# Kernel optimization log

Hardware: AMD Instinct MI355X
Metric: run time of the kernel (lower is better)

The kernel has to match this reference:

```python
import jax, jax.numpy as jnp
import numpy as np

B, L = 1024, 1024
LP, STRIDE, WIN = 64, 32, 8   # patch_length, patch_stride, window_size
GH, RH, NC = 64, 128, 11      # gnn hidden, rnn hidden, num_classes


def setup_inputs() -> dict:
    key = jax.random.key(0)
    ks = jax.random.split(key, 16)
    def n(k, shape, s=0.1):
        return jax.random.normal(k, shape, dtype=jnp.float32) * s
    z = lambda *s: jnp.zeros(s, jnp.float32)
    return {
        "I": jax.random.normal(ks[0], (B, L), dtype=jnp.float32),
        "Q": jax.random.normal(ks[1], (B, L), dtype=jnp.float32),
        "edge_weights": jax.random.normal(ks[2], (LP, LP), dtype=jnp.float32),
        "Wn1": n(ks[3], (GH, 2)),  "bn1": z(GH),
        "Ws1": n(ks[4], (GH, 2)),  "bs1": z(GH),
        "Wn2": n(ks[5], (GH, GH)), "bn2": z(GH),
        "Ws2": n(ks[6], (GH, GH)), "bs2": z(GH),
        "Wih0": n(ks[7], (4 * RH, GH)), "Whh0": n(ks[8], (4 * RH, RH)),
        "bih0": z(4 * RH), "bhh0": z(4 * RH),
        "Wih1": n(ks[9], (4 * RH, RH)), "Whh1": n(ks[10], (4 * RH, RH)),
        "bih1": z(4 * RH), "bhh1": z(4 * RH),
        "Wc1": n(ks[11], (64, RH)), "bc1": z(64),
        "Wc2": n(ks[12], (NC, 64)), "bc2": z(NC),
    }


def _sage(x, adj, deg_inv, Wn, bn, Ws, bs):
    # x: [B,P,Lp,d]; adj: [Lp,Lp]; mean-aggregate neighbors then self+neigh linear + relu
    neigh = jnp.einsum('ij,bpjd->bpid', adj, x) * deg_inv
    return jax.nn.relu(jnp.einsum('bpid,od->bpio', x, Ws) + bs
                       + jnp.einsum('bpid,od->bpio', neigh, Wn) + bn)


def _lstm(x, Wih, Whh, bih, bhh):
    # x: [B,T,D]; PyTorch gate order i,f,g,o
    Hd = Whh.shape[1]
    xg = jnp.einsum('btd,gd->btg', x, Wih) + bih + bhh  # [B,T,4H]
    h0 = jnp.zeros((x.shape[0], Hd), x.dtype)
    def step(carry, xt):
        h, c = carry
        g = xt + h @ Whh.T
        i, f, gg, o = jnp.split(g, 4, axis=-1)
        c = jax.nn.sigmoid(f) * c + jax.nn.sigmoid(i) * jnp.tanh(gg)
        h = jax.nn.sigmoid(o) * jnp.tanh(c)
        return (h, c), h
    (h, _), hs = jax.lax.scan(step, (h0, h0), jnp.swapaxes(xg, 0, 1))
    return jnp.swapaxes(hs, 0, 1), h


def _forward(I, Q, edge_weights, Wn1, bn1, Ws1, bs1, Wn2, bn2, Ws2, bs2,
             Wih0, Whh0, bih0, bhh0, Wih1, Whh1, bih1, bhh1, Wc1, bc1, Wc2, bc2):
    Lp = edge_weights.shape[0]
    P = (I.shape[-1] - Lp) // STRIDE + 1
    # vectorized patch extraction: [B,P,Lp,2]
    idx = jnp.arange(P)[:, None] * STRIDE + jnp.arange(Lp)[None, :]
    patches = jnp.stack([I[:, idx], Q[:, idx]], axis=-1)
    # banded adjacency shared across all patches
    r = jnp.arange(Lp)
    mask = ((jnp.abs(r[:, None] - r[None, :]) <= WIN) & (r[:, None] != r[None, :])).astype(jnp.float32)
    adj = jax.nn.sigmoid(edge_weights) * mask
    deg = adj.sum(axis=1, keepdims=True)           # [Lp,1]
    deg_inv = jnp.where(deg > 0, 1.0 / deg, 0.0)
    x = _sage(patches, adj, deg_inv, Wn1, bn1, Ws1, bs1)   # [B,P,Lp,GH]
    x = _sage(x, adj, deg_inv, Wn2, bn2, Ws2, bs2)
    feats = x.sum(axis=2)                                  # [B,P,GH]
    out0, _ = _lstm(feats, Wih0, Whh0, bih0, bhh0)
    _, h = _lstm(out0, Wih1, Whh1, bih1, bhh1)             # last layer final hidden [B,RH]
    hid = jax.nn.relu(h @ Wc1.T + bc1)
    return hid @ Wc2.T + bc2                               # [B,NC]


def reference(I, Q, edge_weights, Wn1, bn1, Ws1, bs1, Wn2, bn2, Ws2, bs2,
              Wih0, Whh0, bih0, bhh0, Wih1, Whh1, bih1, bhh1, Wc1, bc1, Wc2, bc2):
    return _forward(I, Q, edge_weights, Wn1, bn1, Ws1, bs1, Wn2, bn2, Ws2, bs2,
                    Wih0, Whh0, bih0, bhh0, Wih1, Whh1, bih1, bhh1, Wc1, bc1, Wc2, bc2)
```

## Files before the change

kernel.cpp:

```cpp
#include <hip/hip_runtime.h>
#include <hip/hip_bf16.h>
#include <math.h>

#define L_SZ 1024
#define STRIDE_ 32
#define WIN 8
#define PNUM 31
#define NPATCH 31744
#define SGRID 512

#define X1TS 72
#define CAS  136

typedef __attribute__((ext_vector_type(8))) short short8;
typedef __attribute__((ext_vector_type(4))) short short4v;
typedef __attribute__((ext_vector_type(4))) float f32x4;

#define MFMA16(a, b, c) __builtin_amdgcn_mfma_f32_16x16x32_bf16(a, b, c, 0, 0, 0)

__device__ __forceinline__ void bar_lds() {
    __builtin_amdgcn_sched_barrier(0);
    asm volatile("s_waitcnt lgkmcnt(0)" ::: "memory");
    __builtin_amdgcn_s_barrier();
    __builtin_amdgcn_sched_barrier(0);
}

__device__ __forceinline__ float sigf(float x) { return 1.0f / (1.0f + __expf(-x)); }
__device__ __forceinline__ float tanhfast(float x) {
    float ax = fabsf(x);
    float t = __expf(-2.0f * ax);
    return copysignf((1.0f - t) / (1.0f + t), x);
}
__device__ __forceinline__ short f2bf(float f) {
    __hip_bfloat16 h = __float2bfloat16(f);
    return *reinterpret_cast<short*>(&h);
}
__device__ __forceinline__ float bf2f(short s) {
    __hip_bfloat16 h = *reinterpret_cast<__hip_bfloat16*>(&s);
    return __bfloat162float(h);
}

__global__ void adj_kernel(const float* __restrict__ ew, float* __restrict__ adjn) {
    int i = threadIdx.x;
    if (i >= 64) return;
    float sum = 0.f;
    for (int j = 0; j < 64; ++j) {
        int d = i - j; d = d < 0 ? -d : d;
        float a = (d <= WIN && d != 0) ? sigf(ew[i * 64 + j]) : 0.f;
        sum += a;
    }
    float dinv = (sum > 0.f) ? 1.0f / sum : 0.f;
    for (int j = 0; j < 64; ++j) {
        int d = i - j; d = d < 0 ? -d : d;
        float a = (d <= WIN && d != 0) ? sigf(ew[i * 64 + j]) : 0.f;
        adjn[i * 64 + j] = a * dinv;
    }
}

__global__ void prep_kernel(const float* __restrict__ Wih0, const float* __restrict__ Whh0,
                            const float* __restrict__ Wih1, const float* __restrict__ Whh1,
                            const float* __restrict__ adjn,
                            const float* __restrict__ Ws2, const float* __restrict__ Wn2,
                            short* __restrict__ wihf0G, short* __restrict__ wihf1G,
                            short* __restrict__ adjfG, short* __restrict__ wcatfG,
                            short* __restrict__ whhf0G, short* __restrict__ whhf1G) {
    int bid = blockIdx.x, tid = threadIdx.x;
    if (bid < 32) {
        int t = bid * 256 + tid;
        int f = t >> 6, l = t & 63;
        int hl = f & 1, ks = (f >> 1) & 1, nt = f >> 2;
        int q = l >> 4, l15 = l & 15;
        short8 v;
        #pragma unroll
        for (int e = 0; e < 8; ++e) {
            float src = Wih0[(size_t)(nt * 16 + l15) * 64 + ks * 32 + 8 * q + e];
            short hi = f2bf(src);
            v[e] = hl ? f2bf(src - bf2f(hi)) : hi;
        }
        *(short8*)(wihf0G + (size_t)f * 512 + l * 8) = v;
        return;
    }
    if (bid < 96) {
        int t = (bid - 32) * 256 + tid;
        int f = t >> 6, l = t & 63;
        int hl = f & 1, ks = (f >> 1) & 3, nt = f >> 3;
        int q = l >> 4, l15 = l & 15;
        short8 v;
        #pragma unroll
        for (int e = 0; e < 8; ++e) {
            float src = Wih1[(size_t)(nt * 16 + l15) * 128 + ks * 32 + 8 * q + e];
            short hi = f2bf(src);
            v[e] = hl ? f2bf(src - bf2f(hi)) : hi;
        }
        *(short8*)(wihf1G + (size_t)f * 512 + l * 8) = v;
        return;
    }
    if (bid < 106) {
        int t = (bid - 96) * 256 + tid;
        if (t >= 2432) return;
        int f = t >> 6, l = t & 63;
        int q = l >> 4, l15 = l & 15;
        short8 v;
        if (f < 6) {
            const int ntT[6] = {0, 1, 1, 2, 2, 3};
            const int ksT[6] = {0, 0, 1, 0, 1, 1};
            int row = l15 + 16 * ntT[f], col = 8 * q + 32 * ksT[f];
            #pragma unroll
            for (int e = 0; e < 8; ++e)
                v[e] = f2bf(adjn[row * 64 + col + e]);
            *(short8*)(adjfG + ((size_t)f * 64 + l) * 8) = v;
        } else {
            int fi = f - 6;
            int isLo = fi >= 16;
            int ff = isLo ? fi - 16 : fi;
            int nt = ff >> 2, ks = ff & 3;
            int oo = l15 + 16 * nt;
            #pragma unroll
            for (int e = 0; e < 8; ++e) {
                int k = 32 * ks + 8 * q + e;
                float src = (k < 64) ? Ws2[oo * 64 + k] : Wn2[oo * 64 + (k - 64)];
                short hi = f2bf(src);
                v[e] = isLo ? f2bf(src - bf2f(hi)) : hi;
            }
            *(short8*)(wcatfG + ((size_t)fi * 64 + l) * 8) = v;
        }
        return;
    }
    {
        int layer = (bid < 170) ? 0 : 1;
        int base = layer ? 170 : 106;
        const float* Whh = layer ? Whh1 : Whh0;
        short* dst = layer ? whhf1G : whhf0G;
        int t = (bid - base) * 256 + tid;
        int frag = t >> 6, l = t & 63;
        int hl = frag & 1, ks = (frag >> 1) & 3, NT = frag >> 3;
        int g = NT * 16 + (l & 15);
        int kbase = ks * 32 + (l >> 4) * 8;
        short8 v;
        #pragma unroll
        for (int e = 0; e < 8; ++e) {
            float src = Whh[(size_t)g * 128 + kbase + e];
            short hi = f2bf(src);
            v[e] = hl ? f2bf(src - bf2f(hi)) : hi;
        }
        *(short8*)(dst + (size_t)t * 8) = v;
    }
}

__launch_bounds__(256, 2)
__global__ void sage_mfma(const float* __restrict__ I, const float* __restrict__ Q,
                          const float* __restrict__ adjn,
                          const float* __restrict__ Wn1, const float* __restrict__ bn1,
                          const float* __restrict__ Ws1, const float* __restrict__ bs1,
                          const float* __restrict__ bn2, const float* __restrict__ bs2,
                          const short* __restrict__ adjfG, const short* __restrict__ wcatfG,
                          float* __restrict__ feats) {
    __shared__ __align__(16) short s_x1T[2][64 * X1TS];
    __shared__ __align__(16) short s_cat[2][64 * CAS];

    const int tid = threadIdx.x;
    const int w = tid >> 6, l = tid & 63, q = l >> 4, l15 = l & 15;

    const bool hasKs0 = (w <= 2);
    const bool hasKs1 = (w >= 1);
    const int idx0 = (w == 0) ? 0 : (w == 1 ? 1 : 3);
    const int idx1 = (w == 1) ? 2 : (w == 2 ? 4 : 5);
    short8 adjB0 = {}, adjB1 = {};
    if (hasKs0) adjB0 = *(const short8*)(adjfG + ((size_t)idx0 * 64 + l) * 8);
    if (hasKs1) adjB1 = *(const short8*)(adjfG + ((size_t)idx1 * 64 + l) * 8);

    short8 whf[4], wlf[4];
    #pragma unroll
    for (int ks = 0; ks < 4; ++ks) {
        whf[ks] = *(const short8*)(wcatfG + ((size_t)(w * 4 + ks) * 64 + l) * 8);
        wlf[ks] = *(const short8*)(wcatfG + ((size_t)(w * 4 + ks + 16) * 64 + l) * 8);
    }
    const int oo = l15 + 16 * w;
    const float bo = bs2[oo] + bn2[oo];

    float areg[17];
    #pragma unroll
    for (int d = 0; d < 17; ++d) {
        int j = l + d - WIN;
        areg[d] = (j >= 0 && j < 64) ? adjn[l * 64 + j] : 0.f;
    }

    float x0a[2], x0b[2];
    #pragma unroll
    for (int P = 0; P < 2; ++P) {
        int m = blockIdx.x + P * 512;
        int b = m / PNUM, p = m % PNUM;
        x0a[P] = I[(size_t)b * L_SZ + p * STRIDE_ + l];
        x0b[P] = Q[(size_t)b * L_SZ + p * STRIDE_ + l];
    }

    for (int it = 0; it < 31; ++it) {
        const int m0 = it * 1024 + blockIdx.x;

        #pragma unroll
        for (int P = 0; P < 2; ++P) {
            float n0a = 0.f, n0b = 0.f;
            #pragma unroll
            for (int d = 0; d < 17; ++d) {
                int j = l + d - WIN;
                float xa = __shfl(x0a[P], j, 64);
                float xb = __shfl(x0b[P], j, 64);
                n0a += areg[d] * xa;
                n0b += areg[d] * xb;
            }
            union { short s[16]; short8 v[2]; } pk;
            #pragma unroll
            for (int t = 0; t < 16; ++t) {
                int o = w * 16 + t;
                float2 wsv = ((const float2*)Ws1)[o];
                float2 wnv = ((const float2*)Wn1)[o];
                float v = bs1[o] + bn1[o] + wsv.x * x0a[P] + wsv.y * x0b[P]
                                          + wnv.x * n0a + wnv.y * n0b;
                v = fmaxf(v, 0.f);
                short bv = f2bf(v);
                s_x1T[P][o * X1TS + l] = bv;
                pk.s[t] = bv;
            }
            *(short8*)&s_cat[P][l * CAS + w * 16]     = pk.v[0];
            *(short8*)&s_cat[P][l * CAS + w * 16 + 8] = pk.v[1];
        }

        if (it + 1 < 31) {
            #pragma unroll
            for (int P = 0; P < 2; ++P) {
                int m = (it + 1) * 1024 + blockIdx.x + P * 512;
                int b = m / PNUM, p = m % PNUM;
                x0a[P] = I[(size_t)b * L_SZ + p * STRIDE_ + l];
                x0b[P] = Q[(size_t)b * L_SZ + p * STRIDE_ + l];
            }
        }
        bar_lds();

        #pragma unroll
        for (int P = 0; P < 2; ++P) {
            #pragma unroll
            for (int ot = 0; ot < 4; ++ot) {
                f32x4 c = {0.f, 0.f, 0.f, 0.f};
                if (hasKs0) {
                    short8 a = *(const short8*)&s_x1T[P][(16 * ot + l15) * X1TS + 8 * q];
                    c = MFMA16(a, adjB0, c);
                }
                if (hasKs1) {
                    short8 a = *(const short8*)&s_x1T[P][(16 * ot + l15) * X1TS + 8 * q + 32];
                    c = MFMA16(a, adjB1, c);
                }
                short4v nv;
                nv[0] = f2bf(c[0]); nv[1] = f2bf(c[1]);
                nv[2] = f2bf(c[2]); nv[3] = f2bf(c[3]);
                *(short4v*)&s_cat[P][(16 * w + l15) * CAS + 64 + 16 * ot + 4 * q] = nv;
            }
        }
        bar_lds();

        #pragma unroll
        for (int P = 0; P < 2; ++P) {
            f32x4 z = {0.f, 0.f, 0.f, 0.f};
            f32x4 acc2[4] = {z, z, z, z};
            #pragma unroll
            for (int it2 = 0; it2 < 4; ++it2) {
                short8 a2[4];
                #pragma unroll
                for (int ks = 0; ks < 4; ++ks)
                    a2[ks] = *(const short8*)&s_cat[P][(16 * it2 + l15) * CAS + 32 * ks + 8 * q];
                #pragma unroll
                for (int ks = 0; ks < 4; ++ks) {
                    acc2[it2] = MFMA16(a2[ks], whf[ks], acc2[it2]);
                    acc2[it2] = MFMA16(a2[ks], wlf[ks], acc2[it2]);
                }
            }
            float total = 0.f;
            #pragma unroll
            for (int it2 = 0; it2 < 4; ++it2) {
                float s = fmaxf(acc2[it2][0] + bo, 0.f) + fmaxf(acc2[it2][1] + bo, 0.f)
                        + fmaxf(acc2[it2][2] + bo, 0.f) + fmaxf(acc2[it2][3] + bo, 0.f);
                s += __shfl_xor(s, 16);
                s += __shfl_xor(s, 32);
                total += s;
            }
            if (l < 16)
                feats[(size_t)(m0 + P * 512) * 64 + 16 * w + l15] = total;
        }
        bar_lds();
    }
}

template <int K>
__launch_bounds__(256, 2)
__global__ void gemm_mfma(const float* __restrict__ A, const short* __restrict__ wihfG,
                          const float* __restrict__ bias1, const float* __restrict__ bias2,
                          float* __restrict__ C) {
    constexpr int K32 = K / 32;
    constexpr int K4 = K / 4;
    constexpr int AS = (K == 64) ? 72 : 136;
    __shared__ __align__(16) short s_ah[64 * AS];
    __shared__ __align__(16) short s_al[64 * AS];
    const int tid = threadIdx.x;
    const int w = tid >> 6, l = tid & 63, q = l >> 4, l15 = l & 15;
    const int m0 = blockIdx.x * 64;
    const int j0 = blockIdx.y * 128;

    {
        const float4* Ag = (const float4*)(A + (size_t)m0 * K);
        for (int e = tid; e < 16 * K; e += 256) {
            int row = e / K4, c4 = e % K4;
            float4 v = Ag[row * K4 + c4];
            short4v h, lo;
            h[0] = f2bf(v.x); lo[0] = f2bf(v.x - bf2f(h[0]));
            h[1] = f2bf(v.y); lo[1] = f2bf(v.y - bf2f(h[1]));
            h[2] = f2bf(v.z); lo[2] = f2bf(v.z - bf2f(h[2]));
            h[3] = f2bf(v.w); lo[3] = f2bf(v.w - bf2f(h[3]));
            *(short4v*)&s_ah[row * AS + c4 * 4] = h;
            *(short4v*)&s_al[row * AS + c4 * 4] = lo;
        }
    }

    short8 bh[2][K32], bl[2][K32];
    #pragma unroll
    for (int c = 0; c < 2; ++c) {
        int nt = (j0 >> 4) + 2 * w + c;
        #pragma unroll
        for (int ks = 0; ks < K32; ++ks) {
            bh[c][ks] = *(const short8*)(wihfG + (((size_t)(nt * K32 + ks) * 2 + 0) * 64 + l) * 8);
            bl[c][ks] = *(const short8*)(wihfG + (((size_t)(nt * K32 + ks) * 2 + 1) * 64 + l) * 8);
        }
    }
    __syncthreads();

    f32x4 z = {0.f, 0.f, 0.f, 0.f};
    #pragma unroll
    for (int mt = 0; mt < 4; ++mt) {
        f32x4 acc[2] = {z, z};
        #pragma unroll
        for (int ks = 0; ks < K32; ++ks) {
            short8 ah = *(const short8*)&s_ah[(16 * mt + l15) * AS + 32 * ks + 8 * q];
            short8 al = *(const short8*)&s_al[(16 * mt + l15) * AS + 32 * ks + 8 * q];
            #pragma unroll
            for (int c = 0; c < 2; ++c) {
                acc[c] = MFMA16(ah, bh[c][ks], acc[c]);
                acc[c] = MFMA16(al, bh[c][ks], acc[c]);
                acc[c] = MFMA16(ah, bl[c][ks], acc[c]);
            }
        }
        #pragma unroll
        for (int c = 0; c < 2; ++c) {
            int col = j0 + (2 * w + c) * 16 + l15;
            float bo = bias1[col] + bias2[col];
            #pragma unroll
            for (int reg = 0; reg < 4; ++reg) {
                int row = m0 + 16 * mt + 4 * q + reg;
                C[(size_t)row * 512 + col] = acc[c][reg] + bo;
            }
        }
    }
}

#define HS 136

template <bool FINAL>
__launch_bounds__(512)
__global__ void lstm_mfma(const float* __restrict__ xg, const short* __restrict__ whhfG,
                          float* __restrict__ out0,
                          const float* __restrict__ Wc1, const float* __restrict__ bc1,
                          const float* __restrict__ Wc2, const float* __restrict__ bc2,
                          float* __restrict__ out) {
    __shared__ __align__(16) short s_h[16 * HS];
    __shared__ __align__(16) float s_hid[4 * 68];
    const int tid = threadIdx.x;
    const int w = tid >> 6, l = tid & 63, quad = l >> 4, l15 = l & 15;
    const int b0 = blockIdx.x * 4;
    const int j = 16 * w + l15;
    const int row = quad;

    short8 whf[16], wlf[16];
    #pragma unroll
    for (int nt = 0; nt < 4; ++nt)
        #pragma unroll
        for (int ks = 0; ks < 4; ++ks) {
            size_t NT = (size_t)(w + 8 * nt);
            whf[nt * 4 + ks] = *(const short8*)(whhfG + (((NT * 4 + ks) * 2 + 0) * 64 + l) * 8);
            wlf[nt * 4 + ks] = *(const short8*)(whhfG + (((NT * 4 + ks) * 2 + 1) * 64 + l) * 8);
        }

    float c0 = 0.f;
    for (int e = tid; e < 16 * HS; e += 512) s_h[e] = 0;
    __syncthreads();

    float xgv[4];
    {
        size_t base = ((size_t)(b0 + row) * PNUM + 0) * 512 + j;
        xgv[0] = xg[base];
        xgv[1] = xg[base + 128];
        xgv[2] = xg[base + 256];
        xgv[3] = xg[base + 384];
    }

    for (int t = 0; t < 31; ++t) {
        short8 af[4];
        #pragma unroll
        for (int ks = 0; ks < 4; ++ks)
            af[ks] = *(const short8*)&s_h[l15 * HS + ks * 32 + quad * 8];
        bar_lds();

        f32x4 z = {0.f, 0.f, 0.f, 0.f};
        f32x4 acc[4] = {z, z, z, z};
        #pragma unroll
        for (int nt = 0; nt < 4; ++nt)
            #pragma unroll
            for (int ks = 0; ks < 4; ++ks) {
                acc[nt] = MFMA16(af[ks], whf[nt * 4 + ks], acc[nt]);
                acc[nt] = MFMA16(af[ks], wlf[nt * 4 + ks], acc[nt]);
            }

        float nx0 = 0.f, nx1 = 0.f, nx2 = 0.f, nx3 = 0.f;
        if (t + 1 < 31) {
            size_t base = ((size_t)(b0 + row) * PNUM + (t + 1)) * 512 + j;
            nx0 = xg[base];
            nx1 = xg[base + 128];
            nx2 = xg[base + 256];
            nx3 = xg[base + 384];
        }

        float g4[4];
        #pragma unroll
        for (int nt = 0; nt < 4; ++nt) {
            float s0 = __shfl(acc[nt][0], l15, 64);
            float s1 = __shfl(acc[nt][1], l15, 64);
            float s2 = __shfl(acc[nt][2], l15, 64);
            float s3 = __shfl(acc[nt][3], l15, 64);
            g4[nt] = (quad == 0) ? s0 : (quad == 1) ? s1 : (quad == 2) ? s2 : s3;
        }

        {
            float gi = xgv[0] + g4[0];
            float gf = xgv[1] + g4[1];
            float gg = xgv[2] + g4[2];
            float go = xgv[3] + g4[3];
            float cn = sigf(gf) * c0 + sigf(gi) * tanhfast(gg);
            float h = sigf(go) * tanhfast(cn);
            c0 = cn;
            s_h[row * HS + j] = f2bf(h);
            if (!FINAL)
                out0[((size_t)(b0 + row) * PNUM + t) * 128 + j] = h;
        }
        xgv[0] = nx0; xgv[1] = nx1; xgv[2] = nx2; xgv[3] = nx3;
        bar_lds();
    }

    if (FINAL) {
        if (tid < 256) {
            int rr = tid >> 6, uu = tid & 63;
            float acc = bc1[uu];
            const float* wv = Wc1 + (size_t)uu * 128;
            #pragma unroll 8
            for (int k = 0; k < 128; ++k) acc += wv[k] * bf2f(s_h[rr * HS + k]);
            s_hid[rr * 68 + uu] = fmaxf(acc, 0.f);
        }
        __syncthreads();
        if (tid < 44) {
            int rr = tid / 11, cc = tid % 11;
            float acc = bc2[cc];
            #pragma unroll
            for (int uu = 0; uu < 64; ++uu) acc += Wc2[cc * 64 + uu] * s_hid[rr * 68 + uu];
            out[(size_t)(b0 + rr) * 11 + cc] = acc;
        }
    }
}

extern "C" void kernel_launch(void* const* d_in, const int* in_sizes, int n_in,
                              void* d_out, int out_size, void* d_ws, size_t ws_size,
                              hipStream_t stream) {
    (void)in_sizes; (void)n_in; (void)out_size; (void)ws_size;
    const float* I    = (const float*)d_in[0];
    const float* Q    = (const float*)d_in[1];
    const float* ew   = (const float*)d_in[2];
    const float* Wn1  = (const float*)d_in[3];
    const float* bn1  = (const float*)d_in[4];
    const float* Ws1  = (const float*)d_in[5];
    const float* bs1  = (const float*)d_in[6];
    const float* Wn2  = (const float*)d_in[7];
    const float* bn2  = (const float*)d_in[8];
    const float* Ws2  = (const float*)d_in[9];
    const float* bs2  = (const float*)d_in[10];
    const float* Wih0 = (const float*)d_in[11];
    const float* Whh0 = (const float*)d_in[12];
    const float* bih0 = (const float*)d_in[13];
    const float* bhh0 = (const float*)d_in[14];
    const float* Wih1 = (const float*)d_in[15];
    const float* Whh1 = (const float*)d_in[16];
    const float* bih1 = (const float*)d_in[17];
    const float* bhh1 = (const float*)d_in[18];
    const float* Wc1  = (const float*)d_in[19];
    const float* bc1  = (const float*)d_in[20];
    const float* Wc2  = (const float*)d_in[21];
    const float* bc2  = (const float*)d_in[22];
    float* out = (float*)d_out;

    float* wsp   = (float*)d_ws;
    float* adjn  = wsp;
    short* wihf0G = (short*)(adjn + 4096);
    short* wihf1G = (short*)(adjn + 4096 + 32768);
    short* adjfG  = (short*)(adjn + 4096 + 98304);
    short* wcatfG = adjfG + 3072;
    short* whhf0G = wcatfG + 16384;
    short* whhf1G = whhf0G + 131072;
    float* feats = adjn + 4096 + 98304 + 140800;
    float* out0  = feats + 2031616;
    float* xg    = out0  + 4063232;

    adj_kernel<<<1, 64, 0, stream>>>(ew, adjn);
    prep_kernel<<<234, 256, 0, stream>>>(Wih0, Whh0, Wih1, Whh1, adjn, Ws2, Wn2,
                                         wihf0G, wihf1G, adjfG, wcatfG, whhf0G, whhf1G);
    sage_mfma<<<SGRID, 256, 0, stream>>>(I, Q, adjn, Wn1, bn1, Ws1, bs1,
                                         bn2, bs2, adjfG, wcatfG, feats);
    gemm_mfma<64><<<dim3(496, 4), 256, 0, stream>>>(feats, wihf0G, bih0, bhh0, xg);
    lstm_mfma<false><<<256, 512, 0, stream>>>(xg, whhf0G, out0,
                                              nullptr, nullptr, nullptr, nullptr, nullptr);
    gemm_mfma<128><<<dim3(496, 4), 256, 0, stream>>>(out0, wihf1G, bih1, bhh1, xg);
    lstm_mfma<true><<<256, 512, 0, stream>>>(xg, whhf1G, nullptr,
                                             Wc1, bc1, Wc2, bc2, out);
}
```

Before: 406.3 us.

## Process one patch per iteration in sage kernel with doubled grid and occupancy

```diff
diff --git a/kernel.cpp b/kernel.cpp
--- a/kernel.cpp
+++ b/kernel.cpp
@@ -7,7 +7,7 @@
 #define WIN 8
 #define PNUM 31
 #define NPATCH 31744
-#define SGRID 512
+#define SGRID 1024
 
 #define X1TS 72
 #define CAS  136
@@ -147,7 +147,7 @@
     }
 }
 
-__launch_bounds__(256, 2)
+__launch_bounds__(256, 4)
 __global__ void sage_mfma(const float* __restrict__ I, const float* __restrict__ Q,
                           const float* __restrict__ adjn,
                           const float* __restrict__ Wn1, const float* __restrict__ bn1,
@@ -155,8 +155,8 @@
                           const float* __restrict__ bn2, const float* __restrict__ bs2,
                           const short* __restrict__ adjfG, const short* __restrict__ wcatfG,
                           float* __restrict__ feats) {
-    __shared__ __align__(16) short s_x1T[2][64 * X1TS];
-    __shared__ __align__(16) short s_cat[2][64 * CAS];
+    __shared__ __align__(16) short s_x1T[64 * X1TS];
+    __shared__ __align__(16) short s_cat[64 * CAS];
 
     const int tid = threadIdx.x;
     const int w = tid >> 6, l = tid & 63, q = l >> 4, l15 = l & 15;
@@ -185,26 +185,30 @@
         areg[d] = (j >= 0 && j < 64) ? adjn[l * 64 + j] : 0.f;
     }
 
-    float x0a[2], x0b[2];
-    #pragma unroll
-    for (int P = 0; P < 2; ++P) {
-        int m = blockIdx.x + P * 512;
+    int m = blockIdx.x;
+    float x0a, x0b;
+    {
         int b = m / PNUM, p = m % PNUM;
-        x0a[P] = I[(size_t)b * L_SZ + p * STRIDE_ + l];
-        x0b[P] = Q[(size_t)b * L_SZ + p * STRIDE_ + l];
-    }
-
-    for (int it = 0; it < 31; ++it) {
-        const int m0 = it * 1024 + blockIdx.x;
-
-        #pragma unroll
-        for (int P = 0; P < 2; ++P) {
+        x0a = I[(size_t)b * L_SZ + p * STRIDE_ + l];
+        x0b = Q[(size_t)b * L_SZ + p * STRIDE_ + l];
+    }
+
+    while (m < NPATCH) {
+        const int mn = m + SGRID;
+        float nxa = 0.f, nxb = 0.f;
+        if (mn < NPATCH) {
+            int bn = mn / PNUM, pn = mn % PNUM;
+            nxa = I[(size_t)bn * L_SZ + pn * STRIDE_ + l];
+            nxb = Q[(size_t)bn * L_SZ + pn * STRIDE_ + l];
+        }
+
+        {
             float n0a = 0.f, n0b = 0.f;
             #pragma unroll
             for (int d = 0; d < 17; ++d) {
                 int j = l + d - WIN;
-                float xa = __shfl(x0a[P], j, 64);
-                float xb = __shfl(x0b[P], j, 64);
+                float xa = __shfl(x0a, j, 64);
+                float xb = __shfl(x0b, j, 64);
                 n0a += areg[d] * xa;
                 n0b += areg[d] * xb;
             }
@@ -214,51 +218,37 @@
                 int o = w * 16 + t;
                 float2 wsv = ((const float2*)Ws1)[o];
                 float2 wnv = ((const float2*)Wn1)[o];
-                float v = bs1[o] + bn1[o] + wsv.x * x0a[P] + wsv.y * x0b[P]
+                float v = bs1[o] + bn1[o] + wsv.x * x0a + wsv.y * x0b
                                           + wnv.x * n0a + wnv.y * n0b;
                 v = fmaxf(v, 0.f);
                 short bv = f2bf(v);
-                s_x1T[P][o * X1TS + l] = bv;
+                s_x1T[o * X1TS + l] = bv;
                 pk.s[t] = bv;
             }
-            *(short8*)&s_cat[P][l * CAS + w * 16]     = pk.v[0];
-            *(short8*)&s_cat[P][l * CAS + w * 16 + 8] = pk.v[1];
-        }
-
-        if (it + 1 < 31) {
-            #pragma unroll
-            for (int P = 0; P < 2; ++P) {
-                int m = (it + 1) * 1024 + blockIdx.x + P * 512;
-                int b = m / PNUM, p = m % PNUM;
-                x0a[P] = I[(size_t)b * L_SZ + p * STRIDE_ + l];
-                x0b[P] = Q[(size_t)b * L_SZ + p * STRIDE_ + l];
-            }
+            *(short8*)&s_cat[l * CAS + w * 16]     = pk.v[0];
+            *(short8*)&s_cat[l * CAS + w * 16 + 8] = pk.v[1];
         }
         bar_lds();
 
         #pragma unroll
-        for (int P = 0; P < 2; ++P) {
-            #pragma unroll
-            for (int ot = 0; ot < 4; ++ot) {
-                f32x4 c = {0.f, 0.f, 0.f, 0.f};
-                if (hasKs0) {
-                    short8 a = *(const short8*)&s_x1T[P][(16 * ot + l15) * X1TS + 8 * q];
-                    c = MFMA16(a, adjB0, c);
-                }
-                if (hasKs1) {
-                    short8 a = *(const short8*)&s_x1T[P][(16 * ot + l15) * X1TS + 8 * q + 32];
-                    c = MFMA16(a, adjB1, c);
-                }
-                short4v nv;
-                nv[0] = f2bf(c[0]); nv[1] = f2bf(c[1]);
-                nv[2] = f2bf(c[2]); nv[3] = f2bf(c[3]);
-                *(short4v*)&s_cat[P][(16 * w + l15) * CAS + 64 + 16 * ot + 4 * q] = nv;
-            }
+        for (int ot = 0; ot < 4; ++ot) {
+            f32x4 c = {0.f, 0.f, 0.f, 0.f};
+            if (hasKs0) {
+                short8 a = *(const short8*)&s_x1T[(16 * ot + l15) * X1TS + 8 * q];
+                c = MFMA16(a, adjB0, c);
+            }
+            if (hasKs1) {
+                short8 a = *(const short8*)&s_x1T[(16 * ot + l15) * X1TS + 8 * q + 32];
+                c = MFMA16(a, adjB1, c);
+            }
+            short4v nv;
+            nv[0] = f2bf(c[0]); nv[1] = f2bf(c[1]);
+            nv[2] = f2bf(c[2]); nv[3] = f2bf(c[3]);
+            *(short4v*)&s_cat[(16 * w + l15) * CAS + 64 + 16 * ot + 4 * q] = nv;
         }
         bar_lds();
 
-        #pragma unroll
-        for (int P = 0; P < 2; ++P) {
+        {
             f32x4 z = {0.f, 0.f, 0.f, 0.f};
             f32x4 acc2[4] = {z, z, z, z};
             #pragma unroll
@@ -266,7 +256,7 @@
                 short8 a2[4];
                 #pragma unroll
                 for (int ks = 0; ks < 4; ++ks)
-                    a2[ks] = *(const short8*)&s_cat[P][(16 * it2 + l15) * CAS + 32 * ks + 8 * q];
+                    a2[ks] = *(const short8*)&s_cat[(16 * it2 + l15) * CAS + 32 * ks + 8 * q];
                 #pragma unroll
                 for (int ks = 0; ks < 4; ++ks) {
                     acc2[it2] = MFMA16(a2[ks], whf[ks], acc2[it2]);
@@ -283,9 +273,10 @@
                 total += s;
             }
             if (l < 16)
-                feats[(size_t)(m0 + P * 512) * 64 + 16 * w + l15] = total;
+                feats[(size_t)m * 64 + 16 * w + l15] = total;
         }
         bar_lds();
+        x0a = nxa; x0b = nxb; m = mn;
     }
 }
 
```

New measurement: 755.5 us. 86.0% more time.
